# Kernel tuning notes

Measured on AMD Instinct MI355X. Metric: run time of the kernel, lower is better.

## Reference

```python
import jax, jax.numpy as jnp
import numpy as np

LOG_STD_MAX = 2.0
LOG_STD_MIN = -5.0
LN_EPS = 1e-5


def layer_norm(x, scale, bias):
    mu = jnp.mean(x, axis=-1, keepdims=True)
    var = jnp.var(x, axis=-1, keepdims=True)
    return (x - mu) * jax.lax.rsqrt(var + LN_EPS) * scale + bias


def setup_inputs() -> dict:
    key = jax.random.key(0)
    B, OBS, ACT, H, M, K = 4096, 256, 32, 512, 16, 4
    ks = jax.random.split(key, 8)
    def w(k, shape, fan_in):
        return (jax.random.normal(k, shape, jnp.float32) / np.sqrt(fan_in)).astype(jnp.float32)
    return {
        "x": jax.random.normal(ks[0], (B, OBS), jnp.float32),
        "gate_W": w(ks[1], (OBS, M), OBS),
        "gate_b": jnp.zeros((M,), jnp.float32),
        "fc1_W": w(ks[2], (OBS, H * M), OBS),
        "fc1_b": jnp.zeros((H * M,), jnp.float32),
        "norm1_scale": jnp.ones((H * M,), jnp.float32),
        "norm1_bias": jnp.zeros((H * M,), jnp.float32),
        "fc2_W": w(ks[3], (H * M, H * M), H * M),
        "fc2_b": jnp.zeros((H * M,), jnp.float32),
        "norm2_scale": jnp.ones((H * M,), jnp.float32),
        "norm2_bias": jnp.zeros((H * M,), jnp.float32),
        "mean_W": w(ks[4], (H, ACT), H),
        "mean_b": jnp.zeros((ACT,), jnp.float32),
        "logstd_W": w(ks[5], (H, ACT), H),
        "logstd_b": jnp.zeros((ACT,), jnp.float32),
        "topk": K,
    }


def reference(x, gate_W, gate_b, fc1_W, fc1_b, norm1_scale, norm1_bias,
              fc2_W, fc2_b, norm2_scale, norm2_bias,
              mean_W, mean_b, logstd_W, logstd_b, topk):
    B = x.shape[0]
    M = gate_W.shape[1]
    # gating: softmax -> topk -> renormalize -> scatter into full [B, M] scores
    gate_scores = jax.nn.softmax(x @ gate_W + gate_b, axis=-1)  # [B, M]
    topk_vals, topk_idx = jax.lax.top_k(gate_scores, topk)       # [B, K]
    topk_vals = topk_vals / jnp.sum(topk_vals, axis=-1, keepdims=True)
    scores = jnp.zeros_like(gate_scores).at[jnp.arange(B)[:, None], topk_idx].set(topk_vals)
    # trunk: Linear -> LayerNorm -> ReLU, twice
    h = jax.nn.relu(layer_norm(x @ fc1_W + fc1_b, norm1_scale, norm1_bias))
    h = jax.nn.relu(layer_norm(h @ fc2_W + fc2_b, norm2_scale, norm2_bias))
    # reshape [B, H*M] -> [B, H, M] (expert m = strided slice), weighted MEAN over experts
    h = h.reshape(B, -1, M)                                      # [B, H, M]
    mixed = jnp.einsum('bhm,bm->bh', h, scores) / M              # mean, not sum
    mean = mixed @ mean_W + mean_b
    log_std = jnp.tanh(mixed @ logstd_W + logstd_b)
    log_std = LOG_STD_MIN + 0.5 * (LOG_STD_MAX - LOG_STD_MIN) * (log_std + 1.0)
    return mean, log_std
```

## Files before the change

### kernel.cpp

```cpp
#include <hip/hip_runtime.h>
#include <hip/hip_bf16.h>

typedef unsigned int u32;
typedef unsigned short u16;
typedef __bf16 bf16x8 __attribute__((ext_vector_type(8)));
typedef float f32x4 __attribute__((ext_vector_type(4)));

__device__ __forceinline__ u16 f2b(float f) {
    __bf16 b = (__bf16)f;
    return __builtin_bit_cast(u16, b);
}

__device__ __forceinline__ void gld_lds16(const void* g, void* l) {
    __builtin_amdgcn_global_load_lds(
        (const __attribute__((address_space(1))) u32*)(size_t)g,
        (__attribute__((address_space(3))) u32*)(u32)(size_t)l,
        16, 0, 0);
}

#define BARRIER __builtin_amdgcn_s_barrier()
#define LGKM0 asm volatile("s_waitcnt lgkmcnt(0)" ::: "memory")
#define VMC6 asm volatile("s_waitcnt vmcnt(6)" ::: "memory")
#define VMC0 asm volatile("s_waitcnt vmcnt(0)" ::: "memory")
#define MFMA16(d, a, b) d = __builtin_amdgcn_mfma_f32_16x16x32_bf16(a, b, d, 0, 0, 0)

__global__ __launch_bounds__(256) void cast_bf16_kernel(
    const float* __restrict__ in, u16* __restrict__ out, int n4)
{
    int i = blockIdx.x * 256 + threadIdx.x;
    if (i < n4) {
        float4 f = reinterpret_cast<const float4*>(in)[i];
        u32 lo = (u32)f2b(f.x) | ((u32)f2b(f.y) << 16);
        u32 hi = (u32)f2b(f.z) | ((u32)f2b(f.w) << 16);
        uint2 o; o.x = lo; o.y = hi;
        reinterpret_cast<uint2*>(out)[i] = o;
    }
}

__global__ __launch_bounds__(256) void transpose_cast_kernel(
    const float* __restrict__ in, u16* __restrict__ out, int R, int C)
{
    __shared__ float tile[64][65];
    const int t = threadIdx.x;
    const int c0 = blockIdx.x * 64;
    const int r0 = blockIdx.y * 64;
    #pragma unroll
    for (int i = 0; i < 16; ++i) {
        int idx = t + i * 256;
        int r = idx >> 6, c = idx & 63;
        tile[r][c] = in[(long)(r0 + r) * C + (c0 + c)];
    }
    __syncthreads();
    #pragma unroll
    for (int i = 0; i < 8; ++i) {
        int idx = t + i * 256;
        int rr = idx >> 5;
        int cc = idx & 31;
        u32 p = (u32)f2b(tile[cc * 2 + 0][rr]) | ((u32)f2b(tile[cc * 2 + 1][rr]) << 16);
        *reinterpret_cast<u32*>(&out[(long)(c0 + rr) * R + r0 + cc * 2]) = p;
    }
}

__global__ __launch_bounds__(256) void gate_kernel(
    const float* __restrict__ x, const float* __restrict__ gW,
    const float* __restrict__ gb, const int* __restrict__ topk,
    float* __restrict__ scores)
{
    const int t = threadIdx.x;
    const int row = blockIdx.x * 4 + (t >> 6);
    const int l = t & 63;
    const int m = l & 15;
    const int q = l >> 4;
    const int Kk = *topk;
    const float* xr = x + (long)row * 256;
    float p = 0.f;
    for (int k = q * 64; k < q * 64 + 64; ++k)
        p += xr[k] * gW[k * 16 + m];
    p += __shfl_xor(p, 16);
    p += __shfl_xor(p, 32);
    float logit = p + gb[m];
    float mx = logit;
    #pragma unroll
    for (int d = 1; d < 16; d <<= 1) mx = fmaxf(mx, __shfl_xor(mx, d));
    int rank = 0;
    #pragma unroll
    for (int j = 0; j < 16; ++j) {
        float vj = __shfl(logit, (l & 48) | j);
        rank += (vj > logit) || (vj == logit && j < m);
    }
    bool sel = rank < Kk;
    float e = sel ? expf(logit - mx) : 0.f;
    float ssum = e;
    #pragma unroll
    for (int d = 1; d < 16; d <<= 1) ssum += __shfl_xor(ssum, d);
    if (q == 0) scores[row * 16 + m] = e / ssum;
}


template<int GRAN>
__device__ __forceinline__ void stage_half(
    const u16* __restrict__ src, int ld, int rowbase, int kk,
    u16* ldsregion, int h, int w, int l)
{
    #pragma unroll
    for (int j = 0; j < 2; ++j) {
        const int c = w * 2 + j;
        const int o = c * 1024 + l * 16;
        const int os = o ^ (((o >> 7) & 7) << 4);
        const int pos = o >> 7;
        const int row = ((pos / GRAN) * 2 + h) * GRAN + (pos & (GRAN - 1));
        const u16* g = src + (long)(rowbase + row) * ld + kk + ((os & 127) >> 1);
        gld_lds16(g, ldsregion + c * 512);
    }
}

__device__ __forceinline__ bf16x8 ldfrag(const u16* region, int pos, int col) {
    const int o = (pos * 128 + col * 2) ^ ((pos & 7) << 4);
    return *reinterpret_cast<const bf16x8*>(reinterpret_cast<const char*>(region) + o);
}

template<int CB>
__device__ __forceinline__ void ktile_group(
    const u16* __restrict__ A, int lda, const u16* __restrict__ BT, int ldb,
    int brow, int bcol, int kkA1, int kkR,
    int wr, int wc, int r4, int q8, int w, int l,
    u16 (&lds)[2][4][8192], f32x4 (&acc)[8][4])
{
    bf16x8 aL[4][2], aH[4][2], bL[2][2], bH[2][2];

    #pragma unroll
    for (int m = 0; m < 4; ++m) {
        aL[m][0] = ldfrag(lds[CB][0], wr * 64 + m * 16 + r4, q8);
        aL[m][1] = ldfrag(lds[CB][0], wr * 64 + m * 16 + r4, 32 + q8);
    }
    #pragma unroll
    for (int n = 0; n < 2; ++n) {
        bL[n][0] = ldfrag(lds[CB][2], wc * 32 + n * 16 + r4, q8);
        bL[n][1] = ldfrag(lds[CB][2], wc * 32 + n * 16 + r4, 32 + q8);
    }
    stage_half<64>(A, lda, brow, kkA1, &lds[1 - CB][1][0], 1, w, l);
    BARRIER; LGKM0;
    __builtin_amdgcn_s_setprio(1);
    #pragma unroll
    for (int m = 0; m < 4; ++m)
        #pragma unroll
        for (int n = 0; n < 2; ++n) {
            MFMA16(acc[m][n], aL[m][0], bL[n][0]);
            MFMA16(acc[m][n], aL[m][1], bL[n][1]);
        }
    __builtin_amdgcn_s_setprio(0);
    BARRIER;

    #pragma unroll
    for (int n = 0; n < 2; ++n) {
        bH[n][0] = ldfrag(lds[CB][3], wc * 32 + n * 16 + r4, q8);
        bH[n][1] = ldfrag(lds[CB][3], wc * 32 + n * 16 + r4, 32 + q8);
    }
    stage_half<64>(A, lda, brow, kkR, &lds[CB][0][0], 0, w, l);
    BARRIER; LGKM0;
    __builtin_amdgcn_s_setprio(1);
    #pragma unroll
    for (int m = 0; m < 4; ++m)
        #pragma unroll
        for (int n = 0; n < 2; ++n) {
            MFMA16(acc[m][2 + n], aL[m][0], bH[n][0]);
            MFMA16(acc[m][2 + n], aL[m][1], bH[n][1]);
        }
    __builtin_amdgcn_s_setprio(0);
    BARRIER;

    #pragma unroll
    for (int m = 0; m < 4; ++m) {
        aH[m][0] = ldfrag(lds[CB][1], wr * 64 + m * 16 + r4, q8);
        aH[m][1] = ldfrag(lds[CB][1], wr * 64 + m * 16 + r4, 32 + q8);
    }
    stage_half<32>(BT, ldb, bcol, kkR, &lds[CB][2][0], 0, w, l);
    BARRIER; LGKM0;
    __builtin_amdgcn_s_setprio(1);
    #pragma unroll
    for (int m = 0; m < 4; ++m)
        #pragma unroll
        for (int n = 0; n < 2; ++n) {
            MFMA16(acc[4 + m][2 + n], aH[m][0], bH[n][0]);
            MFMA16(acc[4 + m][2 + n], aH[m][1], bH[n][1]);
        }
    __builtin_amdgcn_s_setprio(0);
    BARRIER;

    stage_half<32>(BT, ldb, bcol, kkR, &lds[CB][3][0], 1, w, l);
    BARRIER;
    __builtin_amdgcn_s_setprio(1);
    #pragma unroll
    for (int m = 0; m < 4; ++m)
        #pragma unroll
        for (int n = 0; n < 2; ++n) {
            MFMA16(acc[4 + m][n], aH[m][0], bL[n][0]);
            MFMA16(acc[4 + m][n], aH[m][1], bL[n][1]);
        }
    __builtin_amdgcn_s_setprio(0);
    VMC6;
    BARRIER;
}

__global__ __launch_bounds__(512, 2) void gemm256(
    const u16* __restrict__ A, int lda,
    const u16* __restrict__ BT, int ldb,
    float* __restrict__ C, int ldc, int K)
{
    __shared__ __align__(16) u16 lds[2][4][8192];
    const int t = threadIdx.x;
    const int w = t >> 6, l = t & 63;
    const int wr = w >> 2, wc = w & 3;
    const int r4 = l & 15, q8 = (l >> 4) * 8;
    const int brow = blockIdx.y * 256, bcol = blockIdx.x * 256;
    const int NT = K >> 6;

    f32x4 acc[8][4];
    #pragma unroll
    for (int m = 0; m < 8; ++m)
        #pragma unroll
        for (int n = 0; n < 4; ++n)
            acc[m][n] = (f32x4){0.f, 0.f, 0.f, 0.f};

    stage_half<64>(A, lda, brow, 0, &lds[0][0][0], 0, w, l);
    stage_half<32>(BT, ldb, bcol, 0, &lds[0][2][0], 0, w, l);
    stage_half<32>(BT, ldb, bcol, 0, &lds[0][3][0], 1, w, l);
    stage_half<64>(A, lda, brow, 0, &lds[0][1][0], 1, w, l);
    stage_half<64>(A, lda, brow, 64, &lds[1][0][0], 0, w, l);
    stage_half<32>(BT, ldb, bcol, 64, &lds[1][2][0], 0, w, l);
    stage_half<32>(BT, ldb, bcol, 64, &lds[1][3][0], 1, w, l);
    VMC6;
    BARRIER;

    for (int i = 0; i < (NT >> 1); ++i) {
        const int U = 2 * i;
        int tV = U + 1;
        int tU2 = U + 2;
        int tV2 = U + 3;
        if (tU2 >= NT) tU2 -= NT;
        if (tV2 >= NT) tV2 -= NT;
        const int kkV = (tV >= NT ? tV - NT : tV) << 6;
        const int kkU2 = tU2 << 6;
        const int kkV2 = tV2 << 6;

        ktile_group<0>(A, lda, BT, ldb, brow, bcol, kkV, kkU2,
                       wr, wc, r4, q8, w, l, lds, acc);
        ktile_group<1>(A, lda, BT, ldb, brow, bcol, kkU2, kkV2,
                       wr, wc, r4, q8, w, l, lds, acc);
    }

    VMC0;

    const int crow0 = (l >> 4) * 4;
    const int ccol = l & 15;
    #pragma unroll
    for (int m = 0; m < 8; ++m) {
        #pragma unroll
        for (int n = 0; n < 4; ++n) {
            int gr = brow + wr * 128 + m * 16 + crow0;
            int gc = bcol + wc * 64 + n * 16 + ccol;
            #pragma unroll
            for (int r = 0; r < 4; ++r)
                C[(long)(gr + r) * ldc + gc] = acc[m][n][r];
        }
    }
}

__global__ __launch_bounds__(256) void ln1_kernel(
    const float* __restrict__ Y, const float* __restrict__ fcb,
    const float* __restrict__ g, const float* __restrict__ be,
    u16* __restrict__ H)
{
    const int N = 8192;
    const int row = blockIdx.x;
    const int t = threadIdx.x;
    const float* y = Y + (long)row * N;
    const int base = t * 32;
    float v[32];
    float s = 0.f, s2 = 0.f;
    #pragma unroll
    for (int j = 0; j < 8; ++j) {
        float4 f = *reinterpret_cast<const float4*>(y + base + j * 4);
        float4 bb = *reinterpret_cast<const float4*>(fcb + base + j * 4);
        float a0 = f.x + bb.x, a1 = f.y + bb.y, a2 = f.z + bb.z, a3 = f.w + bb.w;
        v[j * 4 + 0] = a0; v[j * 4 + 1] = a1; v[j * 4 + 2] = a2; v[j * 4 + 3] = a3;
        s += a0 + a1 + a2 + a3;
        s2 += a0 * a0 + a1 * a1 + a2 * a2 + a3 * a3;
    }
    #pragma unroll
    for (int d = 32; d > 0; d >>= 1) { s += __shfl_down(s, d); s2 += __shfl_down(s2, d); }
    __shared__ float red[8];
    if ((t & 63) == 0) { red[t >> 6] = s; red[4 + (t >> 6)] = s2; }
    __syncthreads();
    s = red[0] + red[1] + red[2] + red[3];
    s2 = red[4] + red[5] + red[6] + red[7];
    float mu = s * (1.f / N);
    float var = s2 * (1.f / N) - mu * mu;
    float rs = rsqrtf(var + 1e-5f);
    __align__(16) u16 o[32];
    #pragma unroll
    for (int i = 0; i < 32; ++i) {
        float z = (v[i] - mu) * rs * g[base + i] + be[base + i];
        o[i] = f2b(fmaxf(z, 0.f));
    }
    u16* h = H + (long)row * N + base;
    #pragma unroll
    for (int j = 0; j < 4; ++j)
        *reinterpret_cast<uint4*>(h + j * 8) = *reinterpret_cast<const uint4*>(&o[j * 8]);
}

__global__ __launch_bounds__(256) void ln2_mix_kernel(
    const float* __restrict__ Y, const float* __restrict__ fcb,
    const float* __restrict__ g, const float* __restrict__ be,
    const float* __restrict__ scores, float* __restrict__ mixed)
{
    const int N = 8192;
    const int row = blockIdx.x;
    const int t = threadIdx.x;
    const float* y = Y + (long)row * N;
    const int base = t * 32;
    __shared__ float sc[16];
    if (t < 16) sc[t] = scores[row * 16 + t];
    float v[32];
    float s = 0.f, s2 = 0.f;
    #pragma unroll
    for (int j = 0; j < 8; ++j) {
        float4 f = *reinterpret_cast<const float4*>(y + base + j * 4);
        float4 bb = *reinterpret_cast<const float4*>(fcb + base + j * 4);
        float a0 = f.x + bb.x, a1 = f.y + bb.y, a2 = f.z + bb.z, a3 = f.w + bb.w;
        v[j * 4 + 0] = a0; v[j * 4 + 1] = a1; v[j * 4 + 2] = a2; v[j * 4 + 3] = a3;
        s += a0 + a1 + a2 + a3;
        s2 += a0 * a0 + a1 * a1 + a2 * a2 + a3 * a3;
    }
    #pragma unroll
    for (int d = 32; d > 0; d >>= 1) { s += __shfl_down(s, d); s2 += __shfl_down(s2, d); }
    __shared__ float red[8];
    if ((t & 63) == 0) { red[t >> 6] = s; red[4 + (t >> 6)] = s2; }
    __syncthreads();
    s = red[0] + red[1] + red[2] + red[3];
    s2 = red[4] + red[5] + red[6] + red[7];
    float mu = s * (1.f / N);
    float var = s2 * (1.f / N) - mu * mu;
    float rs = rsqrtf(var + 1e-5f);
    float m0 = 0.f, m1 = 0.f;
    #pragma unroll
    for (int m = 0; m < 16; ++m) {
        float z0 = fmaxf((v[m] - mu) * rs * g[base + m] + be[base + m], 0.f);
        float z1 = fmaxf((v[16 + m] - mu) * rs * g[base + 16 + m] + be[base + 16 + m], 0.f);
        m0 += z0 * sc[m];
        m1 += z1 * sc[m];
    }
    float2 out; out.x = m0 * (1.f / 16.f); out.y = m1 * (1.f / 16.f);
    *reinterpret_cast<float2*>(&mixed[(long)row * 512 + 2 * t]) = out;
}

__global__ __launch_bounds__(256) void heads_kernel(
    const float* __restrict__ mixed, const float* __restrict__ mW,
    const float* __restrict__ mb, const float* __restrict__ sW,
    const float* __restrict__ sb, float* __restrict__ out)
{
    const int B = 4096;
    const int rb = blockIdx.x * 8;
    const int t = threadIdx.x;
    const int bl = t >> 5;
    const int a = t & 31;
    __shared__ float mx[8][512];
    for (int i = t; i < 8 * 512; i += 256)
        mx[i >> 9][i & 511] = mixed[(long)(rb + (i >> 9)) * 512 + (i & 511)];
    __syncthreads();
    float am = mb[a], as = sb[a];
    for (int h = 0; h < 512; ++h) {
        float xv = mx[bl][h];
        am += xv * mW[h * 32 + a];
        as += xv * sW[h * 32 + a];
    }
    int row = rb + bl;
    out[(long)row * 32 + a] = am;
    float ts = tanhf(as);
    out[(long)B * 32 + (long)row * 32 + a] = -5.0f + 3.5f * (ts + 1.0f);
}

extern "C" void kernel_launch(void* const* d_in, const int* in_sizes, int n_in,
                              void* d_out, int out_size, void* d_ws, size_t ws_size,
                              hipStream_t stream) {
    const float* x   = (const float*)d_in[0];
    const float* gW  = (const float*)d_in[1];
    const float* gb  = (const float*)d_in[2];
    const float* w1  = (const float*)d_in[3];
    const float* b1  = (const float*)d_in[4];
    const float* g1  = (const float*)d_in[5];
    const float* be1 = (const float*)d_in[6];
    const float* w2  = (const float*)d_in[7];
    const float* b2  = (const float*)d_in[8];
    const float* g2  = (const float*)d_in[9];
    const float* be2 = (const float*)d_in[10];
    const float* mW  = (const float*)d_in[11];
    const float* mb  = (const float*)d_in[12];
    const float* sW  = (const float*)d_in[13];
    const float* sb  = (const float*)d_in[14];
    const int* topk  = (const int*)d_in[15];
    float* out = (float*)d_out;

    char* ws = (char*)d_ws;
    u16* W2T = (u16*)ws;            ws += (long)8192 * 8192 * 2;
    float* Y = (float*)ws;          ws += (long)4096 * 8192 * 4;
    u16* H1 = (u16*)ws;             ws += (long)4096 * 8192 * 2;
    u16* W1T = (u16*)ws;            ws += (long)8192 * 256 * 2;
    u16* XB = (u16*)ws;             ws += (long)4096 * 256 * 2;
    float* SCR = (float*)ws;        ws += (long)4096 * 16 * 4;
    float* MIX = (float*)ws;        ws += (long)4096 * 512 * 4;

    cast_bf16_kernel<<<1024, 256, 0, stream>>>(x, XB, 262144);
    transpose_cast_kernel<<<dim3(128, 4), 256, 0, stream>>>(w1, W1T, 256, 8192);
    transpose_cast_kernel<<<dim3(128, 128), 256, 0, stream>>>(w2, W2T, 8192, 8192);
    gate_kernel<<<1024, 256, 0, stream>>>(x, gW, gb, topk, SCR);

    gemm256<<<dim3(32, 16), 512, 0, stream>>>(XB, 256, W1T, 256, Y, 8192, 256);
    ln1_kernel<<<4096, 256, 0, stream>>>(Y, b1, g1, be1, H1);

    gemm256<<<dim3(32, 16), 512, 0, stream>>>(H1, 8192, W2T, 8192, Y, 8192, 8192);
    ln2_mix_kernel<<<4096, 256, 0, stream>>>(Y, b2, g2, be2, SCR, MIX);

    heads_kernel<<<512, 256, 0, stream>>>(MIX, mW, mb, sW, sb, out);
}
```

Measured before the change: 767.7 us.

## Use 32x32 MFMA, bf16 GEMM output, and XCD-aware block remapping

Switches the GEMM inner loop from 16x16x32 to 32x32x16 bf16 MFMA tiles, which cuts the number of LDS fragment reads per FLOP. The GEMM output is stored as bf16 instead of fp32, halving the intermediate Y traffic written by the GEMMs and read back by the layernorm kernels. Block indices are also remapped so each XCD works on a contiguous 8x8 region of tiles, aiming for better L2 reuse. Rounding the pre-LayerNorm activations to bf16 adds precision loss.

```diff
diff --git a/kernel.cpp b/kernel.cpp
--- a/kernel.cpp
+++ b/kernel.cpp
@@ -5,10 +5,15 @@
 typedef unsigned short u16;
 typedef __bf16 bf16x8 __attribute__((ext_vector_type(8)));
 typedef float f32x4 __attribute__((ext_vector_type(4)));
+typedef float f32x16 __attribute__((ext_vector_type(16)));
 
 __device__ __forceinline__ u16 f2b(float f) {
     __bf16 b = (__bf16)f;
     return __builtin_bit_cast(u16, b);
+}
+__device__ __forceinline__ float b2f(u16 v) {
+    u32 x = ((u32)v) << 16;
+    return __builtin_bit_cast(float, x);
 }
 
 __device__ __forceinline__ void gld_lds16(const void* g, void* l) {
@@ -20,9 +25,10 @@
 
 #define BARRIER __builtin_amdgcn_s_barrier()
 #define LGKM0 asm volatile("s_waitcnt lgkmcnt(0)" ::: "memory")
+#define LGKM8 asm volatile("s_waitcnt lgkmcnt(8)" ::: "memory")
 #define VMC6 asm volatile("s_waitcnt vmcnt(6)" ::: "memory")
 #define VMC0 asm volatile("s_waitcnt vmcnt(0)" ::: "memory")
-#define MFMA16(d, a, b) d = __builtin_amdgcn_mfma_f32_16x16x32_bf16(a, b, d, 0, 0, 0)
+#define MFMA32(d, a, b) d = __builtin_amdgcn_mfma_f32_32x32x16_bf16(a, b, d, 0, 0, 0)
 
 __global__ __launch_bounds__(256) void cast_bf16_kernel(
     const float* __restrict__ in, u16* __restrict__ out, int n4)
@@ -123,67 +129,58 @@
 __device__ __forceinline__ void ktile_group(
     const u16* __restrict__ A, int lda, const u16* __restrict__ BT, int ldb,
     int brow, int bcol, int kkA1, int kkR,
-    int wr, int wc, int r4, int q8, int w, int l,
-    u16 (&lds)[2][4][8192], f32x4 (&acc)[8][4])
-{
-    bf16x8 aL[4][2], aH[4][2], bL[2][2], bH[2][2];
-
-    #pragma unroll
-    for (int m = 0; m < 4; ++m) {
-        aL[m][0] = ldfrag(lds[CB][0], wr * 64 + m * 16 + r4, q8);
-        aL[m][1] = ldfrag(lds[CB][0], wr * 64 + m * 16 + r4, 32 + q8);
-    }
-    #pragma unroll
-    for (int n = 0; n < 2; ++n) {
-        bL[n][0] = ldfrag(lds[CB][2], wc * 32 + n * 16 + r4, q8);
-        bL[n][1] = ldfrag(lds[CB][2], wc * 32 + n * 16 + r4, 32 + q8);
-    }
+    int wr, int wc, int lr, int kq, int w, int l,
+    u16 (&lds)[2][4][8192], f32x16 (&acc)[4][2])
+{
+    bf16x8 aL[2][4], aH[2][4], bL[4], bH[4];
+
+    #pragma unroll
+    for (int mt = 0; mt < 2; ++mt)
+        #pragma unroll
+        for (int kb = 0; kb < 4; ++kb)
+            aL[mt][kb] = ldfrag(lds[CB][0], wr * 64 + mt * 32 + lr, kb * 16 + kq);
+    #pragma unroll
+    for (int kb = 0; kb < 4; ++kb)
+        bL[kb] = ldfrag(lds[CB][2], wc * 32 + lr, kb * 16 + kq);
     stage_half<64>(A, lda, brow, kkA1, &lds[1 - CB][1][0], 1, w, l);
+    LGKM8;
     BARRIER; LGKM0;
     __builtin_amdgcn_s_setprio(1);
     #pragma unroll
-    for (int m = 0; m < 4; ++m)
-        #pragma unroll
-        for (int n = 0; n < 2; ++n) {
-            MFMA16(acc[m][n], aL[m][0], bL[n][0]);
-            MFMA16(acc[m][n], aL[m][1], bL[n][1]);
-        }
+    for (int mt = 0; mt < 2; ++mt)
+        #pragma unroll
+        for (int kb = 0; kb < 4; ++kb)
+            MFMA32(acc[mt][0], aL[mt][kb], bL[kb]);
     __builtin_amdgcn_s_setprio(0);
     BARRIER;
 
     #pragma unroll
-    for (int n = 0; n < 2; ++n) {
-        bH[n][0] = ldfrag(lds[CB][3], wc * 32 + n * 16 + r4, q8);
-        bH[n][1] = ldfrag(lds[CB][3], wc * 32 + n * 16 + r4, 32 + q8);
-    }
+    for (int kb = 0; kb < 4; ++kb)
+        bH[kb] = ldfrag(lds[CB][3], wc * 32 + lr, kb * 16 + kq);
     stage_half<64>(A, lda, brow, kkR, &lds[CB][0][0], 0, w, l);
     BARRIER; LGKM0;
     __builtin_amdgcn_s_setprio(1);
     #pragma unroll
-    for (int m = 0; m < 4; ++m)
-        #pragma unroll
-        for (int n = 0; n < 2; ++n) {
-            MFMA16(acc[m][2 + n], aL[m][0], bH[n][0]);
-            MFMA16(acc[m][2 + n], aL[m][1], bH[n][1]);
-        }
+    for (int mt = 0; mt < 2; ++mt)
+        #pragma unroll
+        for (int kb = 0; kb < 4; ++kb)
+            MFMA32(acc[mt][1], aL[mt][kb], bH[kb]);
     __builtin_amdgcn_s_setprio(0);
     BARRIER;
 
     #pragma unroll
-    for (int m = 0; m < 4; ++m) {
-        aH[m][0] = ldfrag(lds[CB][1], wr * 64 + m * 16 + r4, q8);
-        aH[m][1] = ldfrag(lds[CB][1], wr * 64 + m * 16 + r4, 32 + q8);
-    }
+    for (int mt = 0; mt < 2; ++mt)
+        #pragma unroll
+        for (int kb = 0; kb < 4; ++kb)
+            aH[mt][kb] = ldfrag(lds[CB][1], wr * 64 + mt * 32 + lr, kb * 16 + kq);
     stage_half<32>(BT, ldb, bcol, kkR, &lds[CB][2][0], 0, w, l);
     BARRIER; LGKM0;
     __builtin_amdgcn_s_setprio(1);
     #pragma unroll
-    for (int m = 0; m < 4; ++m)
-        #pragma unroll
-        for (int n = 0; n < 2; ++n) {
-            MFMA16(acc[4 + m][2 + n], aH[m][0], bH[n][0]);
-            MFMA16(acc[4 + m][2 + n], aH[m][1], bH[n][1]);
-        }
+    for (int mt = 0; mt < 2; ++mt)
+        #pragma unroll
+        for (int kb = 0; kb < 4; ++kb)
+            MFMA32(acc[2 + mt][1], aH[mt][kb], bH[kb]);
     __builtin_amdgcn_s_setprio(0);
     BARRIER;
 
@@ -191,12 +188,10 @@
     BARRIER;
     __builtin_amdgcn_s_setprio(1);
     #pragma unroll
-    for (int m = 0; m < 4; ++m)
-        #pragma unroll
-        for (int n = 0; n < 2; ++n) {
-            MFMA16(acc[4 + m][n], aH[m][0], bL[n][0]);
-            MFMA16(acc[4 + m][n], aH[m][1], bL[n][1]);
-        }
+    for (int mt = 0; mt < 2; ++mt)
+        #pragma unroll
+        for (int kb = 0; kb < 4; ++kb)
+            MFMA32(acc[2 + mt][0], aH[mt][kb], bL[kb]);
     __builtin_amdgcn_s_setprio(0);
     VMC6;
     BARRIER;
@@ -205,22 +200,27 @@
 __global__ __launch_bounds__(512, 2) void gemm256(
     const u16* __restrict__ A, int lda,
     const u16* __restrict__ BT, int ldb,
-    float* __restrict__ C, int ldc, int K)
+    u16* __restrict__ C, int ldc, int K)
 {
     __shared__ __align__(16) u16 lds[2][4][8192];
     const int t = threadIdx.x;
     const int w = t >> 6, l = t & 63;
     const int wr = w >> 2, wc = w & 3;
-    const int r4 = l & 15, q8 = (l >> 4) * 8;
-    const int brow = blockIdx.y * 256, bcol = blockIdx.x * 256;
+    const int lr = l & 31, kq = (l >> 5) * 8;
+    const int bid = blockIdx.y * 32 + blockIdx.x;
+    const int xcd = bid & 7, within = bid >> 3;
+    const int by = (xcd >> 2) * 8 + (within >> 3);
+    const int bx = (xcd & 3) * 8 + (within & 7);
+    const int brow = by * 256, bcol = bx * 256;
     const int NT = K >> 6;
 
-    f32x4 acc[8][4];
-    #pragma unroll
-    for (int m = 0; m < 8; ++m)
-        #pragma unroll
-        for (int n = 0; n < 4; ++n)
-            acc[m][n] = (f32x4){0.f, 0.f, 0.f, 0.f};
+    f32x16 acc[4][2];
+    #pragma unroll
+    for (int mt = 0; mt < 4; ++mt)
+        #pragma unroll
+        for (int nt = 0; nt < 2; ++nt)
+            #pragma unroll
+            for (int r = 0; r < 16; ++r) acc[mt][nt][r] = 0.f;
 
     stage_half<64>(A, lda, brow, 0, &lds[0][0][0], 0, w, l);
     stage_half<32>(BT, ldb, bcol, 0, &lds[0][2][0], 0, w, l);
@@ -244,48 +244,53 @@
         const int kkV2 = tV2 << 6;
 
         ktile_group<0>(A, lda, BT, ldb, brow, bcol, kkV, kkU2,
-                       wr, wc, r4, q8, w, l, lds, acc);
+                       wr, wc, lr, kq, w, l, lds, acc);
         ktile_group<1>(A, lda, BT, ldb, brow, bcol, kkU2, kkV2,
-                       wr, wc, r4, q8, w, l, lds, acc);
+                       wr, wc, lr, kq, w, l, lds, acc);
     }
 
     VMC0;
 
-    const int crow0 = (l >> 4) * 4;
-    const int ccol = l & 15;
-    #pragma unroll
-    for (int m = 0; m < 8; ++m) {
-        #pragma unroll
-        for (int n = 0; n < 4; ++n) {
-            int gr = brow + wr * 128 + m * 16 + crow0;
-            int gc = bcol + wc * 64 + n * 16 + ccol;
+    const int rbase = 4 * (l >> 5);
+    const int ccol = l & 31;
+    #pragma unroll
+    for (int mt = 0; mt < 4; ++mt) {
+        #pragma unroll
+        for (int nt = 0; nt < 2; ++nt) {
             #pragma unroll
-            for (int r = 0; r < 4; ++r)
-                C[(long)(gr + r) * ldc + gc] = acc[m][n][r];
+            for (int r = 0; r < 16; ++r) {
+                int gr = brow + wr * 128 + mt * 32 + (r & 3) + 8 * (r >> 2) + rbase;
+                int gc = bcol + wc * 64 + nt * 32 + ccol;
+                C[(long)gr * ldc + gc] = f2b(acc[mt][nt][r]);
+            }
         }
     }
 }
 
 __global__ __launch_bounds__(256) void ln1_kernel(
-    const float* __restrict__ Y, const float* __restrict__ fcb,
+    const u16* __restrict__ Y, const float* __restrict__ fcb,
     const float* __restrict__ g, const float* __restrict__ be,
     u16* __restrict__ H)
 {
     const int N = 8192;
     const int row = blockIdx.x;
     const int t = threadIdx.x;
-    const float* y = Y + (long)row * N;
+    const u16* y = Y + (long)row * N;
     const int base = t * 32;
     float v[32];
     float s = 0.f, s2 = 0.f;
     #pragma unroll
-    for (int j = 0; j < 8; ++j) {
-        float4 f = *reinterpret_cast<const float4*>(y + base + j * 4);
-        float4 bb = *reinterpret_cast<const float4*>(fcb + base + j * 4);
-        float a0 = f.x + bb.x, a1 = f.y + bb.y, a2 = f.z + bb.z, a3 = f.w + bb.w;
-        v[j * 4 + 0] = a0; v[j * 4 + 1] = a1; v[j * 4 + 2] = a2; v[j * 4 + 3] = a3;
-        s += a0 + a1 + a2 + a3;
-        s2 += a0 * a0 + a1 * a1 + a2 * a2 + a3 * a3;
+    for (int j = 0; j < 4; ++j) {
+        uint4 q = *reinterpret_cast<const uint4*>(y + base + j * 8);
+        const u32 ww[4] = {q.x, q.y, q.z, q.w};
+        #pragma unroll
+        for (int e = 0; e < 4; ++e) {
+            float a0 = b2f((u16)(ww[e] & 0xffff)) + fcb[base + j * 8 + e * 2];
+            float a1 = b2f((u16)(ww[e] >> 16)) + fcb[base + j * 8 + e * 2 + 1];
+            v[j * 8 + e * 2] = a0; v[j * 8 + e * 2 + 1] = a1;
+            s += a0 + a1;
+            s2 += a0 * a0 + a1 * a1;
+        }
     }
     #pragma unroll
     for (int d = 32; d > 0; d >>= 1) { s += __shfl_down(s, d); s2 += __shfl_down(s2, d); }
@@ -310,27 +315,31 @@
 }
 
 __global__ __launch_bounds__(256) void ln2_mix_kernel(
-    const float* __restrict__ Y, const float* __restrict__ fcb,
+    const u16* __restrict__ Y, const float* __restrict__ fcb,
     const float* __restrict__ g, const float* __restrict__ be,
     const float* __restrict__ scores, float* __restrict__ mixed)
 {
     const int N = 8192;
     const int row = blockIdx.x;
     const int t = threadIdx.x;
-    const float* y = Y + (long)row * N;
+    const u16* y = Y + (long)row * N;
     const int base = t * 32;
     __shared__ float sc[16];
     if (t < 16) sc[t] = scores[row * 16 + t];
     float v[32];
     float s = 0.f, s2 = 0.f;
     #pragma unroll
-    for (int j = 0; j < 8; ++j) {
-        float4 f = *reinterpret_cast<const float4*>(y + base + j * 4);
-        float4 bb = *reinterpret_cast<const float4*>(fcb + base + j * 4);
-        float a0 = f.x + bb.x, a1 = f.y + bb.y, a2 = f.z + bb.z, a3 = f.w + bb.w;
-        v[j * 4 + 0] = a0; v[j * 4 + 1] = a1; v[j * 4 + 2] = a2; v[j * 4 + 3] = a3;
-        s += a0 + a1 + a2 + a3;
-        s2 += a0 * a0 + a1 * a1 + a2 * a2 + a3 * a3;
+    for (int j = 0; j < 4; ++j) {
+        uint4 q = *reinterpret_cast<const uint4*>(y + base + j * 8);
+        const u32 ww[4] = {q.x, q.y, q.z, q.w};
+        #pragma unroll
+        for (int e = 0; e < 4; ++e) {
+            float a0 = b2f((u16)(ww[e] & 0xffff)) + fcb[base + j * 8 + e * 2];
+            float a1 = b2f((u16)(ww[e] >> 16)) + fcb[base + j * 8 + e * 2 + 1];
+            v[j * 8 + e * 2] = a0; v[j * 8 + e * 2 + 1] = a1;
+            s += a0 + a1;
+            s2 += a0 * a0 + a1 * a1;
+        }
     }
     #pragma unroll
     for (int d = 32; d > 0; d >>= 1) { s += __shfl_down(s, d); s2 += __shfl_down(s2, d); }
@@ -403,7 +412,7 @@
 
     char* ws = (char*)d_ws;
     u16* W2T = (u16*)ws;            ws += (long)8192 * 8192 * 2;
-    float* Y = (float*)ws;          ws += (long)4096 * 8192 * 4;
+    u16* Yb = (u16*)ws;             ws += (long)4096 * 8192 * 2;
     u16* H1 = (u16*)ws;             ws += (long)4096 * 8192 * 2;
     u16* W1T = (u16*)ws;            ws += (long)8192 * 256 * 2;
     u16* XB = (u16*)ws;             ws += (long)4096 * 256 * 2;
@@ -415,11 +424,11 @@
     transpose_cast_kernel<<<dim3(128, 128), 256, 0, stream>>>(w2, W2T, 8192, 8192);
     gate_kernel<<<1024, 256, 0, stream>>>(x, gW, gb, topk, SCR);
 
-    gemm256<<<dim3(32, 16), 512, 0, stream>>>(XB, 256, W1T, 256, Y, 8192, 256);
-    ln1_kernel<<<4096, 256, 0, stream>>>(Y, b1, g1, be1, H1);
-
-    gemm256<<<dim3(32, 16), 512, 0, stream>>>(H1, 8192, W2T, 8192, Y, 8192, 8192);
-    ln2_mix_kernel<<<4096, 256, 0, stream>>>(Y, b2, g2, be2, SCR, MIX);
+    gemm256<<<dim3(32, 16), 512, 0, stream>>>(XB, 256, W1T, 256, Yb, 8192, 256);
+    ln1_kernel<<<4096, 256, 0, stream>>>(Yb, b1, g1, be1, H1);
+
+    gemm256<<<dim3(32, 16), 512, 0, stream>>>(H1, 8192, W2T, 8192, Yb, 8192, 8192);
+    ln2_mix_kernel<<<4096, 256, 0, stream>>>(Yb, b2, g2, be2, SCR, MIX);
 
     heads_kernel<<<512, 256, 0, stream>>>(MIX, mW, mb, sW, sb, out);
 }
```

Measured after the change: 787.4 us. 1.03x slower.
